# Performance work log

Measured on AMD Instinct MI355X. Metric: run time of the kernel, lower is better.

## Reference

```python
import jax, jax.numpy as jnp
import numpy as np
from jax import lax


def setup_inputs() -> dict:
    key = jax.random.key(0)
    k1, k2 = jax.random.split(key)
    B, n = 4096, 64
    logits = jax.random.normal(k1, (B * n, 1), dtype=jnp.float32)
    # teacher (kd) labels; small integer range so adjacent ties actually occur
    kd_labels = jax.random.randint(k2, (B, n), 0, 8, dtype=jnp.int32)
    return {"logits": logits, "kd_labels": kd_labels, "train_n_passages": n}


def _tie_aware_rank_gt(kd_labels):
    # rank_gt[i, j] = 1/(j+1), but ties with the previous passage inherit its value.
    # Equivalent: rank_gt[i, j] = 1/(start_of_group(j) + 1) where groups are runs of
    # equal adjacent kd_labels. Vectorized via cummax over group-start indices.
    B, n = kd_labels.shape
    new_grp = jnp.concatenate(
        [jnp.ones((B, 1), dtype=bool), kd_labels[:, 1:] != kd_labels[:, :-1]], axis=1
    )  # [B, n] True where a new tie-group starts
    pos = jnp.arange(n, dtype=jnp.int32)[None, :]
    start = lax.cummax(jnp.where(new_grp, pos, -1), axis=1)  # index of group start
    return 1.0 / (start.astype(jnp.float32) + 1.0)


def reference(logits, kd_labels, train_n_passages):
    n = train_n_passages
    y_pred = logits.reshape(-1, n)  # [B, n]
    y_true = _tie_aware_rank_gt(kd_labels)  # [B, n]

    # RankNet: all ordered pairs (i, j); keep pairs with true_diff > 0 (targets all 1.0)
    true_diffs = y_true[:, :, None] - y_true[:, None, :]  # [B, n, n]
    pred_diffs = y_pred[:, :, None] - y_pred[:, None, :]  # [B, n, n]
    mask = (true_diffs > 0) & ~jnp.isinf(true_diffs)
    # BCEWithLogits(pred_diff, target=1) = softplus(-pred_diff); mean over masked pairs
    per_pair = jax.nn.softplus(-pred_diffs)
    loss = jnp.sum(jnp.where(mask, per_pair, 0.0)) / jnp.sum(mask).astype(per_pair.dtype)
    return loss
```

## Files before the change

kernel.cpp:

```cpp
#include <hip/hip_runtime.h>
#include <math.h>


#define N 64
#define WPB 4
#define RPW 2
#define LN2 0.6931471805599453f
#define LOG2E 1.4426950408889634f

__device__ __forceinline__ float readlane_f(float v, int srclane) {
    return __int_as_float(__builtin_amdgcn_readlane(__float_as_int(v), srclane));
}

#define TERM(i, p, r) do {                                         \
    const int b_ = bb + (i);                                       \
    float t_  = readlane_f(pa2, b_) - pa2;                         \
    float g_  = __builtin_amdgcn_exp2f(-fabsf(t_));                \
    bool  m_  = b_ > e;                                            \
    float gm_ = m_ ? g_ : 0.0f;                                    \
    p = fmaf(gm_, p, p);                  \
    r += m_ ? fmaxf(t_, 0.0f) : 0.0f;                              \
} while (0)

__global__ __launch_bounds__(256) void rank_loss_fused(
    const float* __restrict__ logits, const int* __restrict__ kd,
    float* __restrict__ out,
    unsigned long long* __restrict__ partials,
    unsigned* __restrict__ gcnt,
    unsigned* __restrict__ root,
    int B, int nb)
{
    const int lane = threadIdx.x & 63;
    const int wave = threadIdx.x >> 6;

    __shared__ float ssum[WPB], scnt[WPB];
    __shared__ int finalizeFlag;
    if (threadIdx.x == 0) finalizeFlag = 0;

    float p0=1.f,p1=1.f,p2=1.f,p3=1.f,p4=1.f,p5=1.f,p6=1.f,p7=1.f;
    float r0=0.f,r1=0.f,r2=0.f,r3=0.f,r4=0.f,r5=0.f,r6=0.f,r7=0.f;
    float cnt = 0.f;

    #pragma unroll
    for (int rr = 0; rr < RPW; ++rr) {
        const int row = (blockIdx.x * WPB + wave) * RPW + rr;
        if (row < B) {
            const int base = row * N + lane;
            const int   k   = kd[base];
            const float pa2 = logits[base] * LOG2E;

            const int knext = __shfl_down(k, 1);
            unsigned long long endm = __ballot(lane == 63 || k != knext);
            const int e = lane + __builtin_ctzll(endm >> lane);
            cnt += (float)(63 - e);

            #pragma unroll 1
            for (int bb = 0; bb < N; bb += 8) {
                TERM(0, p0, r0); TERM(1, p1, r1); TERM(2, p2, r2); TERM(3, p3, r3);
                TERM(4, p4, r4); TERM(5, p5, r5); TERM(6, p6, r6); TERM(7, p7, r7);
            }
        }
    }

    float prod = ((p0 * p1) * (p2 * p3)) * ((p4 * p5) * (p6 * p7));
    float rsum = ((r0 + r1) + (r2 + r3)) + ((r4 + r5) + (r6 + r7));
    float psum = rsum + __builtin_amdgcn_logf(prod);

    #pragma unroll
    for (int off = 32; off; off >>= 1) {
        psum += __shfl_down(psum, off);
        cnt  += __shfl_down(cnt,  off);
    }
    if (lane == 0) { ssum[wave] = psum; scnt[wave] = cnt; }
    __syncthreads();

    if (threadIdx.x == 0) {
        float s = 0.f, c = 0.f;
        #pragma unroll
        for (int w = 0; w < WPB; ++w) { s += ssum[w]; c += scnt[w]; }

        unsigned long long pv =
            ((unsigned long long)__float_as_uint(c) << 32) |
            (unsigned long long)__float_as_uint(s);
        __hip_atomic_store(&partials[blockIdx.x], pv,
                           __ATOMIC_RELAXED, __HIP_MEMORY_SCOPE_AGENT);
        asm volatile("s_waitcnt vmcnt(0)" ::: "memory");

        const unsigned g = (unsigned)blockIdx.x >> 3;
        unsigned go = __hip_atomic_fetch_add(&gcnt[g * 32], 1u,
                           __ATOMIC_RELAXED, __HIP_MEMORY_SCOPE_AGENT);
        if ((go & 7u) == 7u) {
            asm volatile("s_waitcnt vmcnt(0)" ::: "memory");
            unsigned ro = __hip_atomic_fetch_add(root, 1u,
                               __ATOMIC_RELAXED, __HIP_MEMORY_SCOPE_AGENT);
            if ((ro & 63u) == 63u) {
                asm volatile("s_waitcnt vmcnt(0)" ::: "memory");
                finalizeFlag = 1;
            }
        }
    }
    __syncthreads();

    if (finalizeFlag) {
        const int t = threadIdx.x;
        float s = 0.f, c = 0.f;
        #pragma unroll
        for (int j = 0; j < 2; ++j) {
            unsigned long long pv = __hip_atomic_load(&partials[j * 256 + t],
                               __ATOMIC_RELAXED, __HIP_MEMORY_SCOPE_AGENT);
            s += __uint_as_float((unsigned)(pv & 0xffffffffull));
            c += __uint_as_float((unsigned)(pv >> 32));
        }
        #pragma unroll
        for (int off = 32; off; off >>= 1) {
            s += __shfl_down(s, off);
            c += __shfl_down(c, off);
        }
        __shared__ float fs[WPB], fc[WPB];
        if (lane == 0) { fs[wave] = s; fc[wave] = c; }
        __syncthreads();
        if (t == 0) {
            float S = 0.f, C = 0.f;
            #pragma unroll
            for (int w = 0; w < WPB; ++w) { S += fs[w]; C += fc[w]; }
            out[0] = S * LN2 / C;
        }
    }
}

extern "C" void kernel_launch(void* const* d_in, const int* in_sizes, int n_in,
                              void* d_out, int out_size, void* d_ws, size_t ws_size,
                              hipStream_t stream) {
    const float* logits = (const float*)d_in[0];
    const int*   kd     = (const int*)d_in[1];
    float*       out    = (float*)d_out;
    const int B  = in_sizes[1] / N;
    const int nb = B / (WPB * RPW);

    unsigned long long* partials = (unsigned long long*)d_ws;
    unsigned* gcnt = (unsigned*)((char*)d_ws + 8192);
    unsigned* root = (unsigned*)((char*)d_ws + 20480);

    rank_loss_fused<<<nb, 256, 0, stream>>>(logits, kd, out, partials,
                                            gcnt, root, B, nb);
}
```

Measured before the change: 13.15 us.

## Exploit pair symmetry to halve exp evaluations and use 512-thread blocks

Each lane now processes only 32 cyclic offsets instead of all 64 partners. It covers both orientations of each pair using group start and end masks and the identity softplus(-x) = softplus(x) - x, so each unordered pair needs only one exp2. Partner values come from ds_bpermute shuffles instead of readlane broadcasts. Blocks grow to 8 waves, halving the block count, and the tree-reduction thresholds change to match. Shuffles cost more than scalar readlanes, and with fewer blocks the GPU may be less fully occupied.

```diff
diff --git a/kernel.cpp b/kernel.cpp
--- a/kernel.cpp
+++ b/kernel.cpp
@@ -3,26 +3,12 @@
 
 
 #define N 64
-#define WPB 4
+#define WAVES 8
 #define RPW 2
 #define LN2 0.6931471805599453f
 #define LOG2E 1.4426950408889634f
 
-__device__ __forceinline__ float readlane_f(float v, int srclane) {
-    return __int_as_float(__builtin_amdgcn_readlane(__float_as_int(v), srclane));
-}
-
-#define TERM(i, p, r) do {                                         \
-    const int b_ = bb + (i);                                       \
-    float t_  = readlane_f(pa2, b_) - pa2;                         \
-    float g_  = __builtin_amdgcn_exp2f(-fabsf(t_));                \
-    bool  m_  = b_ > e;                                            \
-    float gm_ = m_ ? g_ : 0.0f;                                    \
-    p = fmaf(gm_, p, p);                  \
-    r += m_ ? fmaxf(t_, 0.0f) : 0.0f;                              \
-} while (0)
-
-__global__ __launch_bounds__(256) void rank_loss_fused(
+__global__ __launch_bounds__(512) void rank_loss_fused(
     const float* __restrict__ logits, const int* __restrict__ kd,
     float* __restrict__ out,
     unsigned long long* __restrict__ partials,
@@ -33,37 +19,66 @@
     const int lane = threadIdx.x & 63;
     const int wave = threadIdx.x >> 6;
 
-    __shared__ float ssum[WPB], scnt[WPB];
+    __shared__ float ssum[WAVES], scnt[WAVES];
     __shared__ int finalizeFlag;
     if (threadIdx.x == 0) finalizeFlag = 0;
 
     float p0=1.f,p1=1.f,p2=1.f,p3=1.f,p4=1.f,p5=1.f,p6=1.f,p7=1.f;
-    float r0=0.f,r1=0.f,r2=0.f,r3=0.f,r4=0.f,r5=0.f,r6=0.f,r7=0.f;
+    float rm0=0.f,rm1=0.f,rm2=0.f,rm3=0.f;
+    float rt0=0.f,rt1=0.f,rt2=0.f,rt3=0.f;
     float cnt = 0.f;
 
     #pragma unroll
     for (int rr = 0; rr < RPW; ++rr) {
-        const int row = (blockIdx.x * WPB + wave) * RPW + rr;
+        const int row = (blockIdx.x * WAVES + wave) * RPW + rr;
         if (row < B) {
             const int base = row * N + lane;
             const int   k   = kd[base];
-            const float pa2 = logits[base] * LOG2E;
+            const float pa  = logits[base] * LOG2E;
 
+            const int kprev = __shfl_up(k, 1);
             const int knext = __shfl_down(k, 1);
-            unsigned long long endm = __ballot(lane == 63 || k != knext);
+            const unsigned long long endm   = __ballot(lane == 63 || k != knext);
+            const unsigned long long startm = __ballot(lane == 0  || k != kprev);
             const int e = lane + __builtin_ctzll(endm >> lane);
+            const int s = lane - __builtin_clzll(startm << (63 - lane));
             cnt += (float)(63 - e);
 
-            #pragma unroll 1
-            for (int bb = 0; bb < N; bb += 8) {
-                TERM(0, p0, r0); TERM(1, p1, r1); TERM(2, p2, r2); TERM(3, p3, r3);
-                TERM(4, p4, r4); TERM(5, p5, r5); TERM(6, p6, r6); TERM(7, p7, r7);
+            #pragma unroll 32
+            for (int d = 1; d <= 32; ++d) {
+                const int b  = (lane + d) & 63;
+                const float pb = __shfl(pa, b);
+                const float t  = pb - pa;
+                const float g  = __builtin_amdgcn_exp2f(-fabsf(t));
+                const bool live = (d < 32) | (lane < 32);
+                const bool m1 = (b > e) & live;
+                const bool m2 = (b < s) & live;
+                const bool mne = m1 | m2;
+                const float gm = mne ? g : 0.0f;
+                const float mx = mne ? fmaxf(t, 0.0f) : 0.0f;
+                const float tm = m2 ? t : 0.0f;
+                switch (d & 7) {
+                    case 0: p0 = fmaf(gm, p0, p0); break;
+                    case 1: p1 = fmaf(gm, p1, p1); break;
+                    case 2: p2 = fmaf(gm, p2, p2); break;
+                    case 3: p3 = fmaf(gm, p3, p3); break;
+                    case 4: p4 = fmaf(gm, p4, p4); break;
+                    case 5: p5 = fmaf(gm, p5, p5); break;
+                    case 6: p6 = fmaf(gm, p6, p6); break;
+                    default: p7 = fmaf(gm, p7, p7); break;
+                }
+                switch (d & 3) {
+                    case 0: rm0 += mx; rt0 += tm; break;
+                    case 1: rm1 += mx; rt1 += tm; break;
+                    case 2: rm2 += mx; rt2 += tm; break;
+                    default: rm3 += mx; rt3 += tm; break;
+                }
             }
         }
     }
 
     float prod = ((p0 * p1) * (p2 * p3)) * ((p4 * p5) * (p6 * p7));
-    float rsum = ((r0 + r1) + (r2 + r3)) + ((r4 + r5) + (r6 + r7));
+    float rsum = ((rm0 + rm1) + (rm2 + rm3)) - ((rt0 + rt1) + (rt2 + rt3));
     float psum = rsum + __builtin_amdgcn_logf(prod);
 
     #pragma unroll
@@ -75,13 +90,13 @@
     __syncthreads();
 
     if (threadIdx.x == 0) {
-        float s = 0.f, c = 0.f;
+        float sv = 0.f, cv = 0.f;
         #pragma unroll
-        for (int w = 0; w < WPB; ++w) { s += ssum[w]; c += scnt[w]; }
+        for (int w = 0; w < WAVES; ++w) { sv += ssum[w]; cv += scnt[w]; }
 
         unsigned long long pv =
-            ((unsigned long long)__float_as_uint(c) << 32) |
-            (unsigned long long)__float_as_uint(s);
+            ((unsigned long long)__float_as_uint(cv) << 32) |
+            (unsigned long long)__float_as_uint(sv);
         __hip_atomic_store(&partials[blockIdx.x], pv,
                            __ATOMIC_RELAXED, __HIP_MEMORY_SCOPE_AGENT);
         asm volatile("s_waitcnt vmcnt(0)" ::: "memory");
@@ -93,7 +108,7 @@
             asm volatile("s_waitcnt vmcnt(0)" ::: "memory");
             unsigned ro = __hip_atomic_fetch_add(root, 1u,
                                __ATOMIC_RELAXED, __HIP_MEMORY_SCOPE_AGENT);
-            if ((ro & 63u) == 63u) {
+            if ((ro & 31u) == 31u) {
                 asm volatile("s_waitcnt vmcnt(0)" ::: "memory");
                 finalizeFlag = 1;
             }
@@ -103,26 +118,25 @@
 
     if (finalizeFlag) {
         const int t = threadIdx.x;
-        float s = 0.f, c = 0.f;
-        #pragma unroll
-        for (int j = 0; j < 2; ++j) {
-            unsigned long long pv = __hip_atomic_load(&partials[j * 256 + t],
+        float sv = 0.f, cv = 0.f;
+        if (t < 256) {
+            unsigned long long pv = __hip_atomic_load(&partials[t],
                                __ATOMIC_RELAXED, __HIP_MEMORY_SCOPE_AGENT);
-            s += __uint_as_float((unsigned)(pv & 0xffffffffull));
-            c += __uint_as_float((unsigned)(pv >> 32));
+            sv = __uint_as_float((unsigned)(pv & 0xffffffffull));
+            cv = __uint_as_float((unsigned)(pv >> 32));
         }
         #pragma unroll
         for (int off = 32; off; off >>= 1) {
-            s += __shfl_down(s, off);
-            c += __shfl_down(c, off);
+            sv += __shfl_down(sv, off);
+            cv += __shfl_down(cv, off);
         }
-        __shared__ float fs[WPB], fc[WPB];
-        if (lane == 0) { fs[wave] = s; fc[wave] = c; }
+        __shared__ float fs[WAVES], fc[WAVES];
+        if (lane == 0) { fs[wave] = sv; fc[wave] = cv; }
         __syncthreads();
         if (t == 0) {
             float S = 0.f, C = 0.f;
             #pragma unroll
-            for (int w = 0; w < WPB; ++w) { S += fs[w]; C += fc[w]; }
+            for (int w = 0; w < WAVES; ++w) { S += fs[w]; C += fc[w]; }
             out[0] = S * LN2 / C;
         }
     }
@@ -135,12 +149,12 @@
     const int*   kd     = (const int*)d_in[1];
     float*       out    = (float*)d_out;
     const int B  = in_sizes[1] / N;
-    const int nb = B / (WPB * RPW);
+    const int nb = B / (WAVES * RPW);
 
     unsigned long long* partials = (unsigned long long*)d_ws;
     unsigned* gcnt = (unsigned*)((char*)d_ws + 8192);
-    unsigned* root = (unsigned*)((char*)d_ws + 20480);
+    unsigned* root = (unsigned*)((char*)d_ws + 16384);
 
-    rank_loss_fused<<<nb, 256, 0, stream>>>(logits, kd, out, partials,
-                                            gcnt, root, B, nb);
+    rank_loss_fused<<<nb, WAVES * 64, 0, stream>>>(logits, kd, out, partials,
+                                                   gcnt, root, B, nb);
 }
```

After: 12.22 us. 7.1% less time.
